# Kernel optimization log

Hardware: AMD Instinct MI355X
Metric: run time of the kernel (lower is better)

## Reference

```python
import jax, jax.numpy as jnp
import numpy as np

N_HEAD = 16
N_KV = 4
HEAD_DIM = 128
WINDOW = 1024
SINK = 4
THETA = 10000.0


def _rope_cos_sin(T, dim, theta, dtype):
    inv_freq = 1.0 / (theta ** (jnp.arange(0, dim, 2, dtype=jnp.float32) / dim))
    t = jnp.arange(T, dtype=jnp.float32)
    ang = jnp.outer(t, inv_freq)  # [T, dim/2]
    return jnp.cos(ang).astype(dtype), jnp.sin(ang).astype(dtype)


def _apply_rope(x, cos, sin):
    # x: [B, H, T, D]; cos/sin: [T, D/2]
    d2 = x.shape[-1] // 2
    x1, x2 = x[..., :d2], x[..., d2:]
    return jnp.concatenate([x1 * cos - x2 * sin, x2 * cos + x1 * sin], axis=-1)


def setup_inputs() -> dict:
    key = jax.random.key(0)
    ks = jax.random.split(key, 5)
    B, T, C = 2, 2048, 2048
    x = jax.random.normal(ks[0], (B, T, C), dtype=jnp.float32)
    s = 0.02
    wq = jax.random.normal(ks[1], (C, C), dtype=jnp.float32) * s
    wk = jax.random.normal(ks[2], (N_KV * HEAD_DIM, C), dtype=jnp.float32) * s
    wv = jax.random.normal(ks[3], (N_KV * HEAD_DIM, C), dtype=jnp.float32) * s
    wo = jax.random.normal(ks[4], (C, C), dtype=jnp.float32) * s
    return {"x": x, "wq": wq, "wk": wk, "wv": wv, "wo": wo}


def reference(x, wq, wk, wv, wo):
    B, T, C = x.shape
    # QKV projections (Linear with weight [out, in], no bias)
    q = (x @ wq.T).reshape(B, T, N_HEAD, HEAD_DIM).transpose(0, 2, 1, 3)  # [B,H,T,D]
    k = (x @ wk.T).reshape(B, T, N_KV, HEAD_DIM).transpose(0, 2, 1, 3)    # [B,Hkv,T,D]
    v = (x @ wv.T).reshape(B, T, N_KV, HEAD_DIM).transpose(0, 2, 1, 3)

    cos, sin = _rope_cos_sin(T, HEAD_DIM, THETA, x.dtype)
    q = _apply_rope(q, cos, sin)
    k = _apply_rope(k, cos, sin)

    # GQA: repeat kv heads to match query heads (repeat_interleave on head dim)
    rep = N_HEAD // N_KV
    k = jnp.repeat(k, rep, axis=1)
    v = jnp.repeat(v, rep, axis=1)

    # causal + sliding window + attention sink mask
    i = jnp.arange(T)[:, None]
    j = jnp.arange(T)[None, :]
    allowed = (j <= i) & (((i - j) <= WINDOW) | (j < SINK))
    bias = jnp.where(allowed, 0.0, -jnp.inf).astype(x.dtype)  # [T,T]

    scale = 1.0 / np.sqrt(HEAD_DIM)
    att = jnp.einsum("bhqd,bhkd->bhqk", q, k) * scale + bias
    att = jax.nn.softmax(att, axis=-1)
    y = jnp.einsum("bhqk,bhkd->bhqd", att, v)  # [B,H,T,D]
    y = y.transpose(0, 2, 1, 3).reshape(B, T, C)
    return y @ wo.T
```

## Files before the change

### kernel.cpp

```cpp
#include <hip/hip_runtime.h>
#include <hip/hip_bf16.h>

typedef __bf16 bf16x8 __attribute__((ext_vector_type(8)));
typedef __bf16 bf16x4 __attribute__((ext_vector_type(4)));
typedef float  f32x4  __attribute__((ext_vector_type(4)));
typedef unsigned int uint4v __attribute__((ext_vector_type(4)));

#define NB     2
#define TT     2048
#define CC     2048
#define NH     16
#define NKV    4
#define HD     128
#define WIN    1024
#define SINKN  4
#define QSCALE 0.08838834764831845f

__device__ __forceinline__ void lds_load16(const void* g, void* l) {
    __builtin_amdgcn_global_load_lds(
        (__attribute__((address_space(1))) void*)const_cast<void*>(g),
        (__attribute__((address_space(3))) void*)l, 16, 0, 0);
}

__device__ __forceinline__ unsigned pack2bf(float a, float b) {
    __bf16 x = (__bf16)a, y = (__bf16)b;
    unsigned short ux = __builtin_bit_cast(unsigned short, x);
    unsigned short uy = __builtin_bit_cast(unsigned short, y);
    return (unsigned)ux | ((unsigned)uy << 16);
}

__global__ void prolog_kernel(const float* __restrict__ x,
                              const float* __restrict__ wq, const float* __restrict__ wk,
                              const float* __restrict__ wv, const float* __restrict__ wo,
                              __bf16* __restrict__ xb, __bf16* __restrict__ Wall,
                              float* __restrict__ cosT, float* __restrict__ sinT) {
    const int g = blockIdx.x * 256 + threadIdx.x;
    if (g < 2097152) {
        const int idx = g * 4;
        const float4 v = *(const float4*)(x + idx);
        bf16x4 o;
        o[0] = (__bf16)v.x; o[1] = (__bf16)v.y; o[2] = (__bf16)v.z; o[3] = (__bf16)v.w;
        *(bf16x4*)(xb + idx) = o;
    } else if (g < 4718592) {
        const int idx = (g - 2097152) * 4;
        const float* src; int off;
        if (idx < 4194304)      { src = wq; off = idx; }
        else if (idx < 5242880) { src = wk; off = idx - 4194304; }
        else if (idx < 6291456) { src = wv; off = idx - 5242880; }
        else                    { src = wo; off = idx - 6291456; }
        const float4 v = *(const float4*)(src + off);
        bf16x4 o;
        o[0] = (__bf16)v.x; o[1] = (__bf16)v.y; o[2] = (__bf16)v.z; o[3] = (__bf16)v.w;
        *(bf16x4*)(Wall + idx) = o;
    } else {
        const int i = g - 4718592;
        const int t = i >> 6, d = i & 63;
        const float inv_freq = 1.0f / powf(10000.0f, (float)d * (1.0f / 64.0f));
        const float ang = (float)t * inv_freq;
        cosT[i] = cosf(ang);
        sinT[i] = sinf(ang);
    }
}

__global__ void scatter_vt_kernel(const __bf16* __restrict__ qkv,
                                  const float* __restrict__ cosT,
                                  const float* __restrict__ sinT,
                                  __bf16* __restrict__ Qo,
                                  __bf16* __restrict__ Ko,
                                  __bf16* __restrict__ Vt) {
    __shared__ __bf16 tile[64][72];
    if (blockIdx.x < 2560) {
        const int job = blockIdx.x * 256 + threadIdx.x;
        int m, d8, base_off; __bf16* outp; float scale;
        if (job < 524288) {
            m = job >> 7;
            const int pj = job & 127;
            const int hh = pj >> 3; d8 = pj & 7;
            base_off = hh * 128;
            const int b = m >> 11, t = m & 2047;
            outp = Qo + ((size_t)(b * NH + hh) * TT + t) * HD + d8 * 8;
            scale = QSCALE;
        } else {
            const int j2 = job - 524288;
            m = j2 >> 5;
            const int pj = j2 & 31;
            const int g = pj >> 3; d8 = pj & 7;
            base_off = 2048 + g * 128;
            const int b = m >> 11, t = m & 2047;
            outp = Ko + ((size_t)(b * NKV + g) * TT + t) * HD + d8 * 8;
            scale = 1.0f;
        }
        const int t = m & 2047;
        const __bf16* row = qkv + (size_t)m * 3072 + base_off + d8 * 8;
        const bf16x8 x1 = *(const bf16x8*)row;
        const bf16x8 x2 = *(const bf16x8*)(row + 64);
        const float4 c0 = *(const float4*)(cosT + t * 64 + d8 * 8);
        const float4 c1 = *(const float4*)(cosT + t * 64 + d8 * 8 + 4);
        const float4 s0 = *(const float4*)(sinT + t * 64 + d8 * 8);
        const float4 s1 = *(const float4*)(sinT + t * 64 + d8 * 8 + 4);
        const float cs[8] = {c0.x, c0.y, c0.z, c0.w, c1.x, c1.y, c1.z, c1.w};
        const float sn[8] = {s0.x, s0.y, s0.z, s0.w, s1.x, s1.y, s1.z, s1.w};
        bf16x8 o1, o2;
#pragma unroll
        for (int e = 0; e < 8; ++e) {
            const float a = (float)x1[e], bb = (float)x2[e];
            o1[e] = (__bf16)((a * cs[e] - bb * sn[e]) * scale);
            o2[e] = (__bf16)((bb * cs[e] + a * sn[e]) * scale);
        }
        *(bf16x8*)outp = o1;
        *(bf16x8*)(outp + 64) = o2;
    } else {
        const int idx2 = blockIdx.x - 2560;
        const int t0 = (idx2 & 31) << 6, d0 = ((idx2 >> 5) & 1) << 6, bkv = idx2 >> 6;
        const int b = bkv >> 2, g = bkv & 3;
        const int r = threadIdx.x >> 2, cg = threadIdx.x & 3;
        const __bf16* src = qkv + (size_t)(b * TT + t0 + r) * 3072 + 2560 + g * 128 + d0 + cg * 16;
        *(bf16x8*)&tile[r][cg * 16]     = *(const bf16x8*)src;
        *(bf16x8*)&tile[r][cg * 16 + 8] = *(const bf16x8*)(src + 8);
        __syncthreads();
        __bf16* dst = Vt + ((size_t)bkv * HD + d0 + r) * TT + t0 + cg * 16;
        bf16x8 o0, o1;
#pragma unroll
        for (int c2 = 0; c2 < 8; ++c2) {
            o0[c2] = tile[cg * 16 + c2][r];
            o1[c2] = tile[cg * 16 + 8 + c2][r];
        }
        *(bf16x8*)dst = o0;
        *(bf16x8*)(dst + 8) = o1;
    }
}

template <int OUT_BF16>
__global__ __launch_bounds__(512, 2) void gemm_bt8(const __bf16* __restrict__ A,
                                                   const __bf16* __restrict__ Bm,
                                                   void* __restrict__ C,
                                                   int M, int N, int K) {
    __shared__ __align__(16) __bf16 lA[2][256 * 64];
    __shared__ __align__(16) __bf16 lB[2][256 * 64];
    const int tid = threadIdx.x;
    const int lane = tid & 63;
    const int w = tid >> 6;
    const int wm = w >> 2, wn = w & 3;
    const int nbn = N >> 8;
    const int nwg = (M >> 8) * nbn;
    const int chunk = nwg >> 3;
    const int swz = (blockIdx.x & 7) * chunk + (blockIdx.x >> 3);
    const int bm = swz / nbn, bn = swz % nbn;
    const int m0 = bm << 8, n0 = bn << 8;
    const int lr = lane & 15, lh = lane >> 4;
    const int NT = K >> 6;

    auto stageA = [&](int kt, int buf, int i) {
        const int d = i * 8192 + tid * 16;
        const int row = d >> 7;
        const int colb = (d & 127) ^ ((row & 7) << 4);
        lds_load16(A + (size_t)(m0 + row) * K + kt * 64 + (colb >> 1),
                   (char*)lA[buf] + i * 8192 + w * 1024);
    };
    auto stageB = [&](int kt, int buf, int i) {
        const int d = i * 8192 + tid * 16;
        const int row = d >> 7;
        const int colb = (d & 127) ^ ((row & 7) << 4);
        lds_load16(Bm + (size_t)(n0 + row) * K + kt * 64 + (colb >> 1),
                   (char*)lB[buf] + i * 8192 + w * 1024);
    };

    f32x4 acc[8][4] = {};

#pragma unroll
    for (int i = 0; i < 4; ++i) stageA(0, 0, i);
#pragma unroll
    for (int i = 0; i < 4; ++i) stageB(0, 0, i);
    asm volatile("s_waitcnt vmcnt(0)" ::: "memory");
    __syncthreads();

    for (int kt = 0; kt < NT; ++kt) {
        const int cur = kt & 1, nxt = cur ^ 1;
        const bool pf = (kt + 1 < NT);
        const char* bA = (const char*)lA[cur];
        const char* bB = (const char*)lB[cur];

        bf16x8 aF[4][2], b0[2][2], b1[2][2];
#pragma unroll
        for (int mf = 0; mf < 4; ++mf)
#pragma unroll
            for (int ks = 0; ks < 2; ++ks) {
                const int row = wm * 128 + mf * 16 + lr;
                const int cb = (ks * 64 + lh * 16) ^ ((row & 7) << 4);
                aF[mf][ks] = *(const bf16x8*)(bA + row * 128 + cb);
            }
#pragma unroll
        for (int nf = 0; nf < 2; ++nf)
#pragma unroll
            for (int ks = 0; ks < 2; ++ks) {
                const int row = wn * 64 + nf * 16 + lr;
                const int cb = (ks * 64 + lh * 16) ^ ((row & 7) << 4);
                b0[nf][ks] = *(const bf16x8*)(bB + row * 128 + cb);
            }
        if (pf) { stageA(kt + 1, nxt, 0); stageA(kt + 1, nxt, 1); stageA(kt + 1, nxt, 2); stageA(kt + 1, nxt, 3); }
        __builtin_amdgcn_s_setprio(1);
#pragma unroll
        for (int mf = 0; mf < 4; ++mf)
#pragma unroll
            for (int nf = 0; nf < 2; ++nf)
#pragma unroll
                for (int ks = 0; ks < 2; ++ks)
                    acc[mf][nf] = __builtin_amdgcn_mfma_f32_16x16x32_bf16(aF[mf][ks], b0[nf][ks], acc[mf][nf], 0, 0, 0);
        __builtin_amdgcn_s_setprio(0);

#pragma unroll
        for (int nf = 0; nf < 2; ++nf)
#pragma unroll
            for (int ks = 0; ks < 2; ++ks) {
                const int row = wn * 64 + 32 + nf * 16 + lr;
                const int cb = (ks * 64 + lh * 16) ^ ((row & 7) << 4);
                b1[nf][ks] = *(const bf16x8*)(bB + row * 128 + cb);
            }
        if (pf) { stageB(kt + 1, nxt, 0); stageB(kt + 1, nxt, 1); stageB(kt + 1, nxt, 2); stageB(kt + 1, nxt, 3); }
        __builtin_amdgcn_s_setprio(1);
#pragma unroll
        for (int mf = 0; mf < 4; ++mf)
#pragma unroll
            for (int nf = 0; nf < 2; ++nf)
#pragma unroll
                for (int ks = 0; ks < 2; ++ks)
                    acc[mf][nf + 2] = __builtin_amdgcn_mfma_f32_16x16x32_bf16(aF[mf][ks], b1[nf][ks], acc[mf][nf + 2], 0, 0, 0);
        __builtin_amdgcn_s_setprio(0);

#pragma unroll
        for (int mf = 0; mf < 4; ++mf)
#pragma unroll
            for (int ks = 0; ks < 2; ++ks) {
                const int row = wm * 128 + 64 + mf * 16 + lr;
                const int cb = (ks * 64 + lh * 16) ^ ((row & 7) << 4);
                aF[mf][ks] = *(const bf16x8*)(bA + row * 128 + cb);
            }
        __builtin_amdgcn_s_setprio(1);
#pragma unroll
        for (int mf = 0; mf < 4; ++mf)
#pragma unroll
            for (int nf = 0; nf < 2; ++nf)
#pragma unroll
                for (int ks = 0; ks < 2; ++ks)
                    acc[mf + 4][nf] = __builtin_amdgcn_mfma_f32_16x16x32_bf16(aF[mf][ks], b0[nf][ks], acc[mf + 4][nf], 0, 0, 0);
        __builtin_amdgcn_s_setprio(0);

        __builtin_amdgcn_s_setprio(1);
#pragma unroll
        for (int mf = 0; mf < 4; ++mf)
#pragma unroll
            for (int nf = 0; nf < 2; ++nf)
#pragma unroll
                for (int ks = 0; ks < 2; ++ks)
                    acc[mf + 4][nf + 2] = __builtin_amdgcn_mfma_f32_16x16x32_bf16(aF[mf][ks], b1[nf][ks], acc[mf + 4][nf + 2], 0, 0, 0);
        __builtin_amdgcn_s_setprio(0);

        asm volatile("s_waitcnt vmcnt(0)" ::: "memory");
        __syncthreads();
    }

#pragma unroll
    for (int mf = 0; mf < 8; ++mf)
#pragma unroll
        for (int nf = 0; nf < 4; ++nf)
#pragma unroll
            for (int r = 0; r < 4; ++r) {
                const size_t row = m0 + wm * 128 + mf * 16 + lh * 4 + r;
                const size_t col = n0 + wn * 64 + nf * 16 + lr;
                if (OUT_BF16) ((__bf16*)C)[row * N + col] = (__bf16)acc[mf][nf][r];
                else          ((float*)C)[row * N + col]  = acc[mf][nf][r];
            }
}

template <int OUT_BF16>
__global__ __launch_bounds__(256, 2) void gemm_bt(const __bf16* __restrict__ A,
                                                  const __bf16* __restrict__ Bm,
                                                  void* __restrict__ C,
                                                  int M, int N, int K) {
    __shared__ __align__(16) __bf16 lA[2][128 * 32];
    __shared__ __align__(16) __bf16 lB[2][128 * 32];
    const int tid = threadIdx.x;
    const int lane = tid & 63;
    const int w = tid >> 6;
    const int wr = w >> 1, wc = w & 1;
    const int nbn = N >> 7;
    const int nwg = (M >> 7) * nbn;
    const int chunk = nwg >> 3;
    const int swz = (blockIdx.x & 7) * chunk + (blockIdx.x >> 3);
    const int bm = swz / nbn, bn = swz % nbn;
    const int m0 = bm << 7, n0 = bn << 7;
    const int lr = lane & 15, lk = (lane >> 4) << 3;
    f32x4 acc[4][4] = {};

    auto stage = [&](int k0, int buf) {
#pragma unroll
        for (int L = 0; L < 2; ++L) {
            const int o = L * 4096 + w * 1024 + lane * 16;
            const int row = o >> 6, col = (o & 63) >> 1;
            lds_load16(A + (size_t)(m0 + row) * K + k0 + col, (char*)lA[buf] + L * 4096 + w * 1024);
            lds_load16(Bm + (size_t)(n0 + row) * K + k0 + col, (char*)lB[buf] + L * 4096 + w * 1024);
        }
    };

    stage(0, 0);
    asm volatile("s_waitcnt vmcnt(0)" ::: "memory");
    __syncthreads();

    const int NT = K >> 5;
    for (int kt = 0; kt < NT; ++kt) {
        const int buf = kt & 1;
        if (kt + 1 < NT) stage((kt + 1) << 5, buf ^ 1);

        bf16x8 af[4], bfr[4];
#pragma unroll
        for (int t = 0; t < 4; ++t) {
            af[t]  = *(const bf16x8*)&lA[buf][(wr * 64 + t * 16 + lr) * 32 + lk];
            bfr[t] = *(const bf16x8*)&lB[buf][(wc * 64 + t * 16 + lr) * 32 + lk];
        }
#pragma unroll
        for (int mt = 0; mt < 4; ++mt)
#pragma unroll
            for (int nt = 0; nt < 4; ++nt)
                acc[mt][nt] = __builtin_amdgcn_mfma_f32_16x16x32_bf16(af[mt], bfr[nt], acc[mt][nt], 0, 0, 0);

        asm volatile("s_waitcnt vmcnt(0)" ::: "memory");
        __syncthreads();
    }

    const int r0 = (lane >> 4) * 4;
#pragma unroll
    for (int mt = 0; mt < 4; ++mt)
#pragma unroll
        for (int nt = 0; nt < 4; ++nt)
#pragma unroll
            for (int r = 0; r < 4; ++r) {
                const size_t row = m0 + wr * 64 + mt * 16 + r0 + r;
                const size_t col = n0 + wc * 64 + nt * 16 + lr;
                if (OUT_BF16) ((__bf16*)C)[row * N + col] = (__bf16)acc[mt][nt][r];
                else          ((float*)C)[row * N + col]  = acc[mt][nt][r];
            }
}

__global__ __launch_bounds__(512, 4) void attn_kernel(const __bf16* __restrict__ Q,
                                                      const __bf16* __restrict__ Kg,
                                                      const __bf16* __restrict__ Vt,
                                                      __bf16* __restrict__ Y) {
    const int id = blockIdx.x;
    const int grp = id & 7;
    const int pos = id >> 3;
    const int kv = grp & 3, b = grp >> 2;
    const int qt2 = 63 - pos;
    const int q0 = qt2 << 5;
    const int tid = threadIdx.x, lane = tid & 63, w = tid >> 6;
    const int lr = lane & 15, lh = lane >> 4;
    const int hh = w >> 1;
    const int h  = kv * 4 + hh;
    const int wh = w & 1;

    __shared__ __align__(16) __bf16 lK[2][64 * 128];
    __shared__ __align__(16) __bf16 lV[2][128 * 64];

    bf16x8 qf[4];
    {
        const __bf16* Qb = Q + ((size_t)(b * NH + h) * TT + q0 + wh * 16) * HD;
#pragma unroll
        for (int kc = 0; kc < 4; ++kc)
            qf[kc] = *(const bf16x8*)(Qb + lr * HD + kc * 32 + lh * 8);
    }

    f32x4 acc[8] = {};
    float mrun = -1e30f, lrun = 0.f;
    const int iq = q0 + wh * 16 + lr;

    const __bf16* Kb = Kg + (size_t)(b * NKV + kv) * TT * HD;
    const __bf16* Vb = Vt + (size_t)(b * NKV + kv) * HD * TT;
    const int jend = qt2 >> 1;
    const int jsw  = (q0 > WIN) ? ((q0 - WIN) >> 6) : 0;
    const int jswe = (jsw < 1) ? 1 : jsw;
    const int nv   = (jend >= jswe) ? (jend - jswe + 2) : 1;

    auto stage = [&](int jb, int buf) {
        const int j0s = jb << 6;
#pragma unroll
        for (int L = 0; L < 2; ++L) {
            const int o = L * 8192 + w * 1024 + lane * 16;
            {
                const int row = o >> 8;
                const int colb = (o & 255) ^ ((row & 7) << 4);
                lds_load16(Kb + (size_t)(j0s + row) * HD + (colb >> 1),
                           (char*)lK[buf] + L * 8192 + w * 1024);
            }
            {
                const int row = o >> 7;
                const int colb = (o & 127) ^ ((row & 7) << 4);
                lds_load16(Vb + (size_t)row * TT + j0s + (colb >> 1),
                           (char*)lV[buf] + L * 8192 + w * 1024);
            }
        }
    };

    stage(0, 0);

    for (int idx = 0; idx < nv; ++idx) {
        const int cur = idx & 1;
        const bool pf = (idx + 1 < nv);
        const int jb = (idx == 0) ? 0 : (jswe + idx - 1);
        const int j0 = jb << 6;

        if (pf) stage(jswe + idx, cur ^ 1);
        if (pf) asm volatile("s_waitcnt vmcnt(4)" ::: "memory");
        else    asm volatile("s_waitcnt vmcnt(0)" ::: "memory");
        __builtin_amdgcn_s_barrier();
        __builtin_amdgcn_sched_barrier(0);

        const char* bK = (const char*)lK[cur];
        const char* bV = (const char*)lV[cur];

        f32x4 s4[4];
#pragma unroll
        for (int nt = 0; nt < 4; ++nt) {
            f32x4 s = {0.f, 0.f, 0.f, 0.f};
#pragma unroll
            for (int kc = 0; kc < 4; ++kc) {
                const int row = nt * 16 + lr;
                const int colb = ((kc * 32 + lh * 8) << 1) ^ ((row & 7) << 4);
                const bf16x8 kf = *(const bf16x8*)(bK + row * 256 + colb);
                s = __builtin_amdgcn_mfma_f32_16x16x32_bf16(kf, qf[kc], s, 0, 0, 0);
            }
            s4[nt] = s;
        }

        const bool fullTile = (j0 + 63 <= q0) && (q0 + 31 - j0 <= WIN);
        if (!fullTile) {
#pragma unroll
            for (int nt = 0; nt < 4; ++nt)
#pragma unroll
                for (int r = 0; r < 4; ++r) {
                    const int j = j0 + nt * 16 + lh * 4 + r;
                    const bool ok = (j <= iq) && ((iq - j <= WIN) || (j < SINKN));
                    if (!ok) s4[nt][r] = -1e30f;
                }
        }

        float mx = s4[0][0];
#pragma unroll
        for (int nt = 0; nt < 4; ++nt)
#pragma unroll
            for (int r = 0; r < 4; ++r) mx = fmaxf(mx, s4[nt][r]);
        mx = fmaxf(mx, __shfl_xor(mx, 16, 64));
        mx = fmaxf(mx, __shfl_xor(mx, 32, 64));

        if (!__all(mx - mrun <= 8.0f)) {
            const float mnew = fmaxf(mrun, mx);
            const float corr = __expf(mrun - mnew);
            mrun = mnew;
            lrun *= corr;
#pragma unroll
            for (int r = 0; r < 4; ++r) {
                const float c = __shfl(corr, lh * 4 + r, 64);
#pragma unroll
                for (int dt = 0; dt < 8; ++dt) acc[dt][r] *= c;
            }
        }

        float rsum = 0.f;
#pragma unroll
        for (int nt = 0; nt < 4; ++nt)
#pragma unroll
            for (int r = 0; r < 4; ++r) {
                const float p = __expf(s4[nt][r] - mrun);
                s4[nt][r] = p;
                rsum += p;
            }
        rsum += __shfl_xor(rsum, 16, 64);
        rsum += __shfl_xor(rsum, 32, 64);
        lrun += rsum;

        unsigned pw[4][2];
#pragma unroll
        for (int nt = 0; nt < 4; ++nt) {
            pw[nt][0] = pack2bf(s4[nt][0], s4[nt][1]);
            pw[nt][1] = pack2bf(s4[nt][2], s4[nt][3]);
        }
        bf16x8 pa[2];
#pragma unroll
        for (int kc = 0; kc < 2; ++kc) {
            uint4v wv;
#pragma unroll
            for (int widx = 0; widx < 4; ++widx) {
                const int m = widx & 1;
                const int srcl = lr + 16 * ((2 * lh + (widx >> 1)) & 3);
                const int wA = __shfl((int)pw[2 * kc][m], srcl, 64);
                const int wB = __shfl((int)pw[2 * kc + 1][m], srcl, 64);
                wv[widx] = (unsigned)((lh & 2) ? wB : wA);
            }
            pa[kc] = __builtin_bit_cast(bf16x8, wv);
        }

#pragma unroll
        for (int dt = 0; dt < 8; ++dt) {
#pragma unroll
            for (int kc = 0; kc < 2; ++kc) {
                const int row = dt * 16 + lr;
                const int colb = ((kc * 32 + lh * 8) << 1) ^ ((row & 7) << 4);
                const bf16x8 vf = *(const bf16x8*)(bV + row * 128 + colb);
                acc[dt] = __builtin_amdgcn_mfma_f32_16x16x32_bf16(pa[kc], vf, acc[dt], 0, 0, 0);
            }
        }

        if (pf) __builtin_amdgcn_s_barrier();
    }

    const float inv = 1.f / lrun;
#pragma unroll
    for (int r = 0; r < 4; ++r) {
        const float invr = __shfl(inv, lh * 4 + r, 64);
        const int trow = q0 + wh * 16 + lh * 4 + r;
        __bf16* Yp = Y + ((size_t)b * TT + trow) * CC + h * HD;
#pragma unroll
        for (int dt = 0; dt < 8; ++dt)
            Yp[dt * 16 + lr] = (__bf16)(acc[dt][r] * invr);
    }
}

extern "C" void kernel_launch(void* const* d_in, const int* in_sizes, int n_in,
                              void* d_out, int out_size, void* d_ws, size_t ws_size,
                              hipStream_t stream) {
    const float* x  = (const float*)d_in[0];
    const float* wq = (const float*)d_in[1];
    const float* wk = (const float*)d_in[2];
    const float* wv = (const float*)d_in[3];
    const float* wo = (const float*)d_in[4];
    float* out = (float*)d_out;

    char* ws = (char*)d_ws;
    size_t off = 0;
    auto alloc = [&](size_t bytes) { char* p = ws + off; off += bytes; return p; };
    __bf16* xb   = (__bf16*)alloc(16777216);
    __bf16* Wall = (__bf16*)alloc(12582912);
    __bf16* wob  = (__bf16*)alloc(8388608);
    __bf16* qkv  = (__bf16*)alloc(25165824);
    __bf16* Qs   = (__bf16*)alloc(16777216);
    __bf16* Ks   = (__bf16*)alloc(4194304);
    __bf16* Vts  = (__bf16*)alloc(4194304);
    float*  cosT = (float*)alloc(524288);
    float*  sinT = (float*)alloc(524288);
    __bf16* Yb = xb;

    prolog_kernel<<<18944, 256, 0, stream>>>(x, wq, wk, wv, wo, xb, Wall, cosT, sinT);
    gemm_bt8<1><<<dim3(16 * 12), 512, 0, stream>>>(xb, Wall, qkv, 4096, 3072, 2048);
    scatter_vt_kernel<<<3072, 256, 0, stream>>>(qkv, cosT, sinT, Qs, Ks, Vts);
    attn_kernel<<<dim3(512), 512, 0, stream>>>(Qs, Ks, Vts, Yb);
    gemm_bt<0><<<dim3(32 * 16), 256, 0, stream>>>(Yb, wob, out, 4096, 2048, 2048);
}
```

Before: 176.1 us.

## Fold log2e into Q scale, widen GEMM K-tile with swizzle, single-buffer attention

New measurement: 168.0 us. 1.05x faster.

```diff
diff --git a/kernel.cpp b/kernel.cpp
--- a/kernel.cpp
+++ b/kernel.cpp
@@ -14,7 +14,7 @@
 #define HD     128
 #define WIN    1024
 #define SINKN  4
-#define QSCALE 0.08838834764831845f
+#define QSCALE2 (0.08838834764831845f * 1.44269504088896340f)
 
 __device__ __forceinline__ void lds_load16(const void* g, void* l) {
     __builtin_amdgcn_global_load_lds(
@@ -27,6 +27,12 @@
     unsigned short ux = __builtin_bit_cast(unsigned short, x);
     unsigned short uy = __builtin_bit_cast(unsigned short, y);
     return (unsigned)ux | ((unsigned)uy << 16);
+}
+
+__device__ __forceinline__ float fast_exp2(float x) {
+    float r;
+    asm("v_exp_f32 %0, %1" : "=v"(r) : "v"(x));
+    return r;
 }
 
 __global__ void prolog_kernel(const float* __restrict__ x,
@@ -79,7 +85,7 @@
             base_off = hh * 128;
             const int b = m >> 11, t = m & 2047;
             outp = Qo + ((size_t)(b * NH + hh) * TT + t) * HD + d8 * 8;
-            scale = QSCALE;
+            scale = QSCALE2;
         } else {
             const int j2 = job - 524288;
             m = j2 >> 5;
@@ -277,8 +283,8 @@
                                                   const __bf16* __restrict__ Bm,
                                                   void* __restrict__ C,
                                                   int M, int N, int K) {
-    __shared__ __align__(16) __bf16 lA[2][128 * 32];
-    __shared__ __align__(16) __bf16 lB[2][128 * 32];
+    __shared__ __align__(16) __bf16 lA[2][128 * 64];
+    __shared__ __align__(16) __bf16 lB[2][128 * 64];
     const int tid = threadIdx.x;
     const int lane = tid & 63;
     const int w = tid >> 6;
@@ -289,16 +295,19 @@
     const int swz = (blockIdx.x & 7) * chunk + (blockIdx.x >> 3);
     const int bm = swz / nbn, bn = swz % nbn;
     const int m0 = bm << 7, n0 = bn << 7;
-    const int lr = lane & 15, lk = (lane >> 4) << 3;
+    const int lr = lane & 15, lh = lane >> 4;
     f32x4 acc[4][4] = {};
 
     auto stage = [&](int k0, int buf) {
 #pragma unroll
-        for (int L = 0; L < 2; ++L) {
-            const int o = L * 4096 + w * 1024 + lane * 16;
-            const int row = o >> 6, col = (o & 63) >> 1;
-            lds_load16(A + (size_t)(m0 + row) * K + k0 + col, (char*)lA[buf] + L * 4096 + w * 1024);
-            lds_load16(Bm + (size_t)(n0 + row) * K + k0 + col, (char*)lB[buf] + L * 4096 + w * 1024);
+        for (int i = 0; i < 4; ++i) {
+            const int d = i * 4096 + tid * 16;
+            const int row = d >> 7;
+            const int colb = (d & 127) ^ ((row & 7) << 4);
+            lds_load16(A + (size_t)(m0 + row) * K + k0 + (colb >> 1),
+                       (char*)lA[buf] + i * 4096 + w * 1024);
+            lds_load16(Bm + (size_t)(n0 + row) * K + k0 + (colb >> 1),
+                       (char*)lB[buf] + i * 4096 + w * 1024);
         }
     };
 
@@ -306,22 +315,32 @@
     asm volatile("s_waitcnt vmcnt(0)" ::: "memory");
     __syncthreads();
 
-    const int NT = K >> 5;
+    const int NT = K >> 6;
     for (int kt = 0; kt < NT; ++kt) {
         const int buf = kt & 1;
-        if (kt + 1 < NT) stage((kt + 1) << 5, buf ^ 1);
-
-        bf16x8 af[4], bfr[4];
-#pragma unroll
-        for (int t = 0; t < 4; ++t) {
-            af[t]  = *(const bf16x8*)&lA[buf][(wr * 64 + t * 16 + lr) * 32 + lk];
-            bfr[t] = *(const bf16x8*)&lB[buf][(wc * 64 + t * 16 + lr) * 32 + lk];
-        }
+        if (kt + 1 < NT) stage((kt + 1) << 6, buf ^ 1);
+
+        const char* bA = (const char*)lA[buf];
+        const char* bB = (const char*)lB[buf];
+        bf16x8 af[4][2], bfr[4][2];
+#pragma unroll
+        for (int t = 0; t < 4; ++t)
+#pragma unroll
+            for (int ks = 0; ks < 2; ++ks) {
+                const int rowa = wr * 64 + t * 16 + lr;
+                const int cba = (ks * 64 + lh * 16) ^ ((rowa & 7) << 4);
+                af[t][ks] = *(const bf16x8*)(bA + rowa * 128 + cba);
+                const int rowb = wc * 64 + t * 16 + lr;
+                const int cbb = (ks * 64 + lh * 16) ^ ((rowb & 7) << 4);
+                bfr[t][ks] = *(const bf16x8*)(bB + rowb * 128 + cbb);
+            }
 #pragma unroll
         for (int mt = 0; mt < 4; ++mt)
 #pragma unroll
             for (int nt = 0; nt < 4; ++nt)
-                acc[mt][nt] = __builtin_amdgcn_mfma_f32_16x16x32_bf16(af[mt], bfr[nt], acc[mt][nt], 0, 0, 0);
+#pragma unroll
+                for (int ks = 0; ks < 2; ++ks)
+                    acc[mt][nt] = __builtin_amdgcn_mfma_f32_16x16x32_bf16(af[mt][ks], bfr[nt][ks], acc[mt][nt], 0, 0, 0);
 
         asm volatile("s_waitcnt vmcnt(0)" ::: "memory");
         __syncthreads();
@@ -357,8 +376,8 @@
     const int h  = kv * 4 + hh;
     const int wh = w & 1;
 
-    __shared__ __align__(16) __bf16 lK[2][64 * 128];
-    __shared__ __align__(16) __bf16 lV[2][128 * 64];
+    __shared__ __align__(16) __bf16 lK[64 * 128];
+    __shared__ __align__(16) __bf16 lV[128 * 64];
 
     bf16x8 qf[4];
     {
@@ -376,45 +395,27 @@
     const __bf16* Vb = Vt + (size_t)(b * NKV + kv) * HD * TT;
     const int jend = qt2 >> 1;
     const int jsw  = (q0 > WIN) ? ((q0 - WIN) >> 6) : 0;
-    const int jswe = (jsw < 1) ? 1 : jsw;
-    const int nv   = (jend >= jswe) ? (jend - jswe + 2) : 1;
-
-    auto stage = [&](int jb, int buf) {
-        const int j0s = jb << 6;
+
+    for (int jb = 0; jb <= jend; ++jb) {
+        if (jb > 0 && jb < jsw) continue;
+        const int j0 = jb << 6;
+        __syncthreads();
 #pragma unroll
         for (int L = 0; L < 2; ++L) {
             const int o = L * 8192 + w * 1024 + lane * 16;
             {
                 const int row = o >> 8;
                 const int colb = (o & 255) ^ ((row & 7) << 4);
-                lds_load16(Kb + (size_t)(j0s + row) * HD + (colb >> 1),
-                           (char*)lK[buf] + L * 8192 + w * 1024);
+                lds_load16(Kb + (size_t)(j0 + row) * HD + (colb >> 1), (char*)lK + L * 8192 + w * 1024);
             }
             {
                 const int row = o >> 7;
                 const int colb = (o & 127) ^ ((row & 7) << 4);
-                lds_load16(Vb + (size_t)row * TT + j0s + (colb >> 1),
-                           (char*)lV[buf] + L * 8192 + w * 1024);
-            }
-        }
-    };
-
-    stage(0, 0);
-
-    for (int idx = 0; idx < nv; ++idx) {
-        const int cur = idx & 1;
-        const bool pf = (idx + 1 < nv);
-        const int jb = (idx == 0) ? 0 : (jswe + idx - 1);
-        const int j0 = jb << 6;
-
-        if (pf) stage(jswe + idx, cur ^ 1);
-        if (pf) asm volatile("s_waitcnt vmcnt(4)" ::: "memory");
-        else    asm volatile("s_waitcnt vmcnt(0)" ::: "memory");
-        __builtin_amdgcn_s_barrier();
-        __builtin_amdgcn_sched_barrier(0);
-
-        const char* bK = (const char*)lK[cur];
-        const char* bV = (const char*)lV[cur];
+                lds_load16(Vb + (size_t)row * TT + j0 + (colb >> 1), (char*)lV + L * 8192 + w * 1024);
+            }
+        }
+        asm volatile("s_waitcnt vmcnt(0)" ::: "memory");
+        __syncthreads();
 
         f32x4 s4[4];
 #pragma unroll
@@ -424,7 +425,7 @@
             for (int kc = 0; kc < 4; ++kc) {
                 const int row = nt * 16 + lr;
                 const int colb = ((kc * 32 + lh * 8) << 1) ^ ((row & 7) << 4);
-                const bf16x8 kf = *(const bf16x8*)(bK + row * 256 + colb);
+                const bf16x8 kf = *(const bf16x8*)((const char*)lK + row * 256 + colb);
                 s = __builtin_amdgcn_mfma_f32_16x16x32_bf16(kf, qf[kc], s, 0, 0, 0);
             }
             s4[nt] = s;
@@ -450,9 +451,9 @@
         mx = fmaxf(mx, __shfl_xor(mx, 16, 64));
         mx = fmaxf(mx, __shfl_xor(mx, 32, 64));
 
-        if (!__all(mx - mrun <= 8.0f)) {
+        if (!__all(mx - mrun <= 11.53f)) {
             const float mnew = fmaxf(mrun, mx);
-            const float corr = __expf(mrun - mnew);
+            const float corr = fast_exp2(mrun - mnew);
             mrun = mnew;
             lrun *= corr;
 #pragma unroll
@@ -468,7 +469,7 @@
         for (int nt = 0; nt < 4; ++nt)
 #pragma unroll
             for (int r = 0; r < 4; ++r) {
-                const float p = __expf(s4[nt][r] - mrun);
+                const float p = fast_exp2(s4[nt][r] - mrun);
                 s4[nt][r] = p;
                 rsum += p;
             }
@@ -503,12 +504,10 @@
             for (int kc = 0; kc < 2; ++kc) {
                 const int row = dt * 16 + lr;
                 const int colb = ((kc * 32 + lh * 8) << 1) ^ ((row & 7) << 4);
-                const bf16x8 vf = *(const bf16x8*)(bV + row * 128 + colb);
+                const bf16x8 vf = *(const bf16x8*)((const char*)lV + row * 128 + colb);
                 acc[dt] = __builtin_amdgcn_mfma_f32_16x16x32_bf16(pa[kc], vf, acc[dt], 0, 0, 0);
             }
         }
-
-        if (pf) __builtin_amdgcn_s_barrier();
     }
 
     const float inv = 1.f / lrun;
```
